# Performance work log

Measured on AMD Instinct MI355X. Metric: run time of the kernel, lower is better.

Reference implementation:

```python
import jax, jax.numpy as jnp
import numpy as np

B, S, D = 2, 2048, 2048
H = 16
Q_LORA = 1024
KV_LORA = 512
NOPE = 128
ROPE = 64
VH = 128
QK = NOPE + ROPE
EPS = 1e-3
SCALE = QK ** -0.5


def rms_norm(x, w):
    x32 = x.astype(jnp.float32)
    n = x32 * jax.lax.rsqrt(jnp.mean(x32 * x32, axis=-1, keepdims=True) + EPS)
    return w * n.astype(x.dtype)


def apply_rope(x, cos, sin):
    # x: [b, s, h, d]; cos/sin: [1, s, 1, d//2].
    # torch view_as_complex pairs consecutive elements: (x0,x1),(x2,x3),...
    xr, xi = x[..., 0::2], x[..., 1::2]
    yr = xr * cos - xi * sin
    yi = xr * sin + xi * cos
    return jnp.stack([yr, yi], axis=-1).reshape(x.shape)


def setup_inputs() -> dict:
    key = jax.random.key(0)
    ks = jax.random.split(key, 8)

    def lin(k, out, inn):
        bound = 1.0 / float(np.sqrt(inn))
        return jax.random.uniform(k, (out, inn), jnp.float32, -bound, bound)

    inv_freq = 1.0 / (10000.0 ** (np.arange(0, ROPE, 2, dtype=np.float32) / ROPE))
    ang = np.arange(S, dtype=np.float32)[:, None] * inv_freq[None, :]  # [S, ROPE/2]
    return {
        "x": jax.random.normal(ks[0], (B, S, D), jnp.float32),
        "start_pos": 0,
        "cos": jnp.asarray(np.cos(ang), jnp.float32),
        "sin": jnp.asarray(np.sin(ang), jnp.float32),
        "wq_a_w": lin(ks[1], Q_LORA, D),
        "wq_a_b": jnp.zeros((Q_LORA,), jnp.float32),
        "q_norm_w": jnp.ones((Q_LORA,), jnp.float32),
        "wq_b_w": lin(ks[2], H * QK, Q_LORA),
        "wq_b_b": jnp.zeros((H * QK,), jnp.float32),
        "wkv_a_w": lin(ks[3], KV_LORA + ROPE, D),
        "wkv_a_b": jnp.zeros((KV_LORA + ROPE,), jnp.float32),
        "kv_norm_w": jnp.ones((KV_LORA,), jnp.float32),
        "wkv_b_w": lin(ks[4], H * (NOPE + VH), KV_LORA),
        "wo_w": lin(ks[5], D, H * VH),
        "wo_b": jnp.zeros((D,), jnp.float32),
    }


def reference(x, start_pos, cos, sin, wq_a_w, wq_a_b, q_norm_w, wq_b_w, wq_b_b,
              wkv_a_w, wkv_a_b, kv_norm_w, wkv_b_w, wo_w, wo_b):
    b, s, _ = x.shape
    cos_ = cos[None, :, None, :]
    sin_ = sin[None, :, None, :]

    # q path: low-rank down-proj, RMSNorm, up-proj
    q = rms_norm(x @ wq_a_w.T + wq_a_b, q_norm_w) @ wq_b_w.T + wq_b_b
    q = q.reshape(b, s, H, QK)
    q_nope, q_pe = q[..., :NOPE], q[..., NOPE:]
    q_pe = apply_rope(q_pe, cos_, sin_)

    # kv path: joint low-rank latent + rope key
    kv_full = x @ wkv_a_w.T + wkv_a_b
    kv, k_pe = kv_full[..., :KV_LORA], kv_full[..., KV_LORA:]
    k_pe = apply_rope(k_pe[:, :, None, :], cos_, sin_)[:, :, 0, :]  # [b, t, ROPE]

    wkv_b = wkv_b_w.reshape(H, NOPE + VH, KV_LORA)
    # absorb k up-projection into q (MLA trick): q_nope -> latent space
    q_nope = jnp.einsum('bshd,hdc->bshc', q_nope, wkv_b[:, :NOPE])  # [b,s,H,KV_LORA]

    kv_c = rms_norm(kv, kv_norm_w)  # latent KV cache contents [b, t, KV_LORA]

    scores = (jnp.einsum('bshc,btc->bsht', q_nope, kv_c)
              + jnp.einsum('bshr,btr->bsht', q_pe, k_pe)) * SCALE
    # NOTE: source builds a causal mask but never adds it -> plain softmax (faithful)
    probs = jax.nn.softmax(scores.astype(jnp.float32), axis=-1).astype(x.dtype)

    o = jnp.einsum('bsht,btc->bshc', probs, kv_c)          # latent output
    o = jnp.einsum('bshc,hdc->bshd', o, wkv_b[:, NOPE:])    # v up-projection
    return o.reshape(b, s, H * VH) @ wo_w.T + wo_b
```

## Files before the change

kernel.cpp:

```cpp
#include <hip/hip_runtime.h>
#include <stdint.h>

typedef uint16_t u16;
typedef __bf16 bf16x8 __attribute__((ext_vector_type(8)));
typedef float f32x4 __attribute__((ext_vector_type(4)));
typedef u16 u16x8 __attribute__((ext_vector_type(8)));

#define EPS 1e-3f
#define SCALE_F 0.07216878364870323f
#define SCALE_L2E 0.104117546f
#define THR_RAW 110.0f

__device__ __forceinline__ float bf2f(u16 u) {
    union { uint32_t i; float f; } v; v.i = ((uint32_t)u) << 16; return v.f;
}
__device__ __forceinline__ u16 f2bf(float f) {
    union { float f; uint32_t i; } v; v.f = f;
    uint32_t x = v.i;
    return (u16)((x + 0x7fffu + ((x >> 16) & 1u)) >> 16);
}

__device__ __forceinline__ void async_cp16(const u16* g, u16* l) {
    __builtin_amdgcn_global_load_lds(
        (const __attribute__((address_space(1))) uint32_t*)g,
        (__attribute__((address_space(3))) uint32_t*)l,
        16, 0, 0);
}

struct Cvt {
    const void* src[14];
    u16* dst[14];
    long off[15];
};

__global__ __launch_bounds__(256) void cvt_kernel(Cvt c, const uint32_t* qnw_u32, long total8)
{
    const long i8 = (long)blockIdx.x * 256 + threadIdx.x;
    if (i8 >= total8) return;
    const long e = i8 * 8;
    const bool is_f32 = (qnw_u32[0] == 0x3F800000u);
    int t = 0;
    while (e >= c.off[t + 1]) ++t;
    const long local = e - c.off[t];
    u16* d = c.dst[t] + local;
    if (is_f32) {
        const float* s = (const float*)c.src[t] + local;
        const f32x4 a = *(const f32x4*)s;
        const f32x4 b = *(const f32x4*)(s + 4);
        u16x8 o;
        #pragma unroll
        for (int j = 0; j < 4; ++j) { o[j] = f2bf(a[j]); o[j + 4] = f2bf(b[j]); }
        *(u16x8*)d = o;
    } else {
        *(u16x8*)d = *(const u16x8*)((const u16*)c.src[t] + local);
    }
}

struct GemmP {
    const u16* A; const u16* B; const u16* bias; u16* C;
    int M, N, K, lda, ldb, ldc; float alpha; int c_f32;
    int z0, hcnt;
    long sAl, sAb, sAh, sBl, sBb, sBh, sCl, sCb, sCh;
    int gx, gy;
};

__device__ __forceinline__ void gemm_body(
    u16* As, u16* Bs, int bx, int by, int bz, const GemmP& p)
{
    const u16* A = p.A; const u16* B = p.B; const u16* bias = p.bias;
    u16* C = p.C;
    const int N = p.N, K = p.K, lda = p.lda, ldb = p.ldb, ldc = p.ldc;

    const int zg = p.z0 + bz;
    const int zb = zg / p.hcnt, zh = zg - zb * p.hcnt;
    A += (long)bz * p.sAl + (long)zb * p.sAb + (long)zh * p.sAh;
    B += (long)bz * p.sBl + (long)zb * p.sBb + (long)zh * p.sBh;
    C += (long)bz * p.sCl + (long)zb * p.sCb + (long)zh * p.sCh;

    const int tid  = threadIdx.x;
    const int wave = tid >> 6, lane = tid & 63;
    const int wm = (wave >> 1) << 6, wn = (wave & 1) << 6;
    const int quad = lane >> 4, r15 = lane & 15;

    const int tileM = by * 128;
    const int tileN = bx * 128;

    const u16* Ag[4]; const u16* Bg[4];
    u16* lA[4]; u16* lB[4];
    #pragma unroll
    for (int i = 0; i < 4; ++i) {
        const int cc = i * 256 + tid;
        const int rA = cc >> 3, kb = (cc & 7) << 3;
        int rB = tileN + rA; if (rB > N - 1) rB = N - 1;
        Ag[i] = A + (long)(tileM + rA) * lda + kb;
        Bg[i] = B + (long)rB * ldb + kb;
        lA[i] = &As[cc << 3];
        lB[i] = &Bs[cc << 3];
    }

    f32x4 acc[4][4] = {};

    const u16* aRd[4]; const u16* bRd[4];
    #pragma unroll
    for (int i = 0; i < 4; ++i) {
        aRd[i] = &As[(wm + i * 16 + r15) * 64 + quad * 8];
        bRd[i] = &Bs[(wn + i * 16 + r15) * 64 + quad * 8];
    }

    for (int k0 = 0; k0 < K; k0 += 64) {
        #pragma unroll
        for (int i = 0; i < 4; ++i) {
            async_cp16(Ag[i], lA[i]);
            async_cp16(Bg[i], lB[i]);
            Ag[i] += 64; Bg[i] += 64;
        }
        __syncthreads();
        #pragma unroll
        for (int kk = 0; kk < 2; ++kk) {
            bf16x8 af[4], bfr[4];
            #pragma unroll
            for (int i = 0; i < 4; ++i) {
                af[i]  = *(const bf16x8*)(aRd[i] + kk * 32);
                bfr[i] = *(const bf16x8*)(bRd[i] + kk * 32);
            }
            #pragma unroll
            for (int mi = 0; mi < 4; ++mi)
                #pragma unroll
                for (int ni = 0; ni < 4; ++ni)
                    acc[mi][ni] = __builtin_amdgcn_mfma_f32_16x16x32_bf16(
                        af[mi], bfr[ni], acc[mi][ni], 0, 0, 0);
        }
        __syncthreads();
    }

    #pragma unroll
    for (int mi = 0; mi < 4; ++mi) {
        const int row = tileM + wm + mi * 16 + quad * 4;
        #pragma unroll
        for (int ni = 0; ni < 4; ++ni) {
            const int col = tileN + wn + ni * 16 + r15;
            if (col < N) {
                if (p.c_f32) {
                    const float bv = bias ? bf2f(bias[col]) : 0.f;
                    #pragma unroll
                    for (int r = 0; r < 4; ++r)
                        ((float*)C)[(long)(row + r) * ldc + col] =
                            acc[mi][ni][r] * p.alpha + bv;
                } else {
                    #pragma unroll
                    for (int r = 0; r < 4; ++r) {
                        u16 t = f2bf(acc[mi][ni][r] * p.alpha);
                        if (bias) t = f2bf(bf2f(t) + bf2f(bias[col]));
                        C[(long)(row + r) * ldc + col] = t;
                    }
                }
            }
        }
    }
}

__global__ __launch_bounds__(256) void gemm_bt_kernel(GemmP p)
{
    __shared__ u16 As[128 * 64];
    __shared__ u16 Bs[128 * 64];
    gemm_body(As, Bs, blockIdx.x, blockIdx.y, blockIdx.z, p);
}

__global__ __launch_bounds__(256) void gemm_dual_kernel(GemmP pa, GemmP pb, int na)
{
    __shared__ u16 As[128 * 64];
    __shared__ u16 Bs[128 * 64];
    int bid = blockIdx.x;
    if (bid < na) {
        const int bx = bid % pa.gx; const int rem = bid / pa.gx;
        gemm_body(As, Bs, bx, rem % pa.gy, rem / pa.gy, pa);
    } else {
        bid -= na;
        const int bx = bid % pb.gx; const int rem = bid / pb.gx;
        gemm_body(As, Bs, bx, rem % pb.gy, rem / pb.gy, pb);
    }
}

#define PS 72

__global__ __launch_bounds__(256, 2) void flash_kernel(
    const u16* __restrict__ q, const u16* __restrict__ K2,
    const u16* __restrict__ Vt, u16* __restrict__ O,
    const u16* __restrict__ cosb, const u16* __restrict__ sinb)
{
    __shared__ __align__(16) u16 Ks[64 * 192];
    __shared__ __align__(16) u16 Vs[128 * 64];
    __shared__ __align__(16) u16 Ps[4][32 * PS];

    const int bid = blockIdx.x;
    const int xcd = bid & 7;
    const int idx = bid >> 3;
    const int bh  = xcd * 4 + (idx >> 4);
    const int mt  = idx & 15;
    const int b = bh >> 4, h = bh & 15;

    const int tid = threadIdx.x;
    const int wave = tid >> 6, lane = tid & 63;
    const int quad = lane >> 4, r15 = lane & 15;
    const int r7 = r15 & 7;

    const long qrow0 = (long)b * 2048 + mt * 128 + wave * 32;
    u16* myPs = Ps[wave];

    bf16x8 qf[2][6];
    #pragma unroll
    for (int mi = 0; mi < 2; ++mi) {
        const u16* qp = q + (qrow0 + mi * 16 + r15) * 3072 + h * 192 + quad * 8;
        #pragma unroll
        for (int kst = 0; kst < 4; ++kst)
            qf[mi][kst] = *(const bf16x8*)(qp + kst * 32);
        const int srow = mt * 128 + wave * 32 + mi * 16 + r15;
        #pragma unroll
        for (int kst = 4; kst < 6; ++kst) {
            const u16x8 v = *(const u16x8*)(qp + kst * 32);
            u16x8 o;
            const int jj0 = (kst - 4) * 16 + quad * 4;
            #pragma unroll
            for (int pp = 0; pp < 4; ++pp) {
                const float xr = bf2f(v[2 * pp]), xi = bf2f(v[2 * pp + 1]);
                const float c  = bf2f(cosb[(long)srow * 32 + jj0 + pp]);
                const float si = bf2f(sinb[(long)srow * 32 + jj0 + pp]);
                o[2 * pp]     = f2bf(bf2f(f2bf(xr * c))  - bf2f(f2bf(xi * si)));
                o[2 * pp + 1] = f2bf(bf2f(f2bf(xr * si)) + bf2f(f2bf(xi * c)));
            }
            qf[mi][kst] = *(const bf16x8*)&o;
        }
    }

    f32x4 Oacc[2][8] = {};
    float m_i[2][4], l_i[2][4];
    #pragma unroll
    for (int mi = 0; mi < 2; ++mi)
        #pragma unroll
        for (int r = 0; r < 4; ++r) { m_i[mi][r] = -1e30f; l_i[mi][r] = 0.f; }

    const u16* Kbh = K2 + (long)b * 2048 * 3072 + h * 192;
    const u16* Vbh = Vt + (long)bh * 128 * 2048;

    const u16* gK[6];
    #pragma unroll
    for (int i = 0; i < 6; ++i) {
        const int c = i * 256 + tid;
        const int row = c / 24, s = c - row * 24;
        gK[i] = Kbh + (long)row * 3072 + ((s ^ (row & 7)) << 3);
    }
    const u16* gV[4];
    #pragma unroll
    for (int i = 0; i < 4; ++i) {
        const int c = i * 256 + tid;
        const int d = c >> 3, s = c & 7;
        gV[i] = Vbh + (long)d * 2048 + ((s ^ (d & 7)) << 3);
    }

    #pragma unroll
    for (int i = 0; i < 6; ++i) {
        async_cp16(gK[i], &Ks[(i * 256 + tid) << 3]);
        gK[i] += 64 * 3072;
    }
    __syncthreads();

    for (int j = 0; j < 32; ++j) {
        #pragma unroll
        for (int i = 0; i < 4; ++i) {
            async_cp16(gV[i], &Vs[(i * 256 + tid) << 3]);
            gV[i] += 64;
        }

        f32x4 S[2][4] = {};
        __builtin_amdgcn_s_setprio(1);
        #pragma unroll
        for (int kst = 0; kst < 6; ++kst) {
            bf16x8 bfr[4];
            #pragma unroll
            for (int ni = 0; ni < 4; ++ni)
                bfr[ni] = *(const bf16x8*)&Ks[(ni * 16 + r15) * 192
                                              + (((kst * 4 + quad) ^ r7) << 3)];
            #pragma unroll
            for (int mi = 0; mi < 2; ++mi)
                #pragma unroll
                for (int ni = 0; ni < 4; ++ni)
                    S[mi][ni] = __builtin_amdgcn_mfma_f32_16x16x32_bf16(
                        qf[mi][kst], bfr[ni], S[mi][ni], 0, 0, 0);
        }
        __builtin_amdgcn_s_setprio(0);

        __syncthreads();

        #pragma unroll
        for (int i = 0; i < 6; ++i) {
            async_cp16(gK[i], &Ks[(i * 256 + tid) << 3]);
            gK[i] += 64 * 3072;
        }

        float tmax[2][4];
        float gmax = -1e30f;
        #pragma unroll
        for (int mi = 0; mi < 2; ++mi)
            #pragma unroll
            for (int r = 0; r < 4; ++r) {
                float t = fmaxf(fmaxf(S[mi][0][r], S[mi][1][r]),
                                fmaxf(S[mi][2][r], S[mi][3][r]));
                t = fmaxf(t, __shfl_xor(t, 1, 16));
                t = fmaxf(t, __shfl_xor(t, 2, 16));
                t = fmaxf(t, __shfl_xor(t, 4, 16));
                t = fmaxf(t, __shfl_xor(t, 8, 16));
                tmax[mi][r] = t;
                gmax = fmaxf(gmax, t - m_i[mi][r]);
            }
        if (!__all(gmax <= THR_RAW)) {
            #pragma unroll
            for (int mi = 0; mi < 2; ++mi)
                #pragma unroll
                for (int r = 0; r < 4; ++r) {
                    const float mnew = fmaxf(m_i[mi][r], tmax[mi][r]);
                    const float al = exp2f((m_i[mi][r] - mnew) * SCALE_L2E);
                    m_i[mi][r] = mnew;
                    l_i[mi][r] *= al;
                    #pragma unroll
                    for (int ni = 0; ni < 8; ++ni) Oacc[mi][ni][r] *= al;
                }
        }
        #pragma unroll
        for (int mi = 0; mi < 2; ++mi)
            #pragma unroll
            for (int r = 0; r < 4; ++r) {
                const int lrow = mi * 16 + quad * 4 + r;
                const float mm = m_i[mi][r];
                float ps = 0.f;
                #pragma unroll
                for (int ni = 0; ni < 4; ++ni) {
                    const float pv = exp2f((S[mi][ni][r] - mm) * SCALE_L2E);
                    ps += pv;
                    myPs[lrow * PS + ni * 16 + r15] = f2bf(pv);
                }
                ps += __shfl_xor(ps, 1, 16);
                ps += __shfl_xor(ps, 2, 16);
                ps += __shfl_xor(ps, 4, 16);
                ps += __shfl_xor(ps, 8, 16);
                l_i[mi][r] += ps;
            }

        __builtin_amdgcn_s_setprio(1);
        #pragma unroll
        for (int kst = 0; kst < 2; ++kst) {
            bf16x8 af[2], bv[8];
            #pragma unroll
            for (int mi = 0; mi < 2; ++mi)
                af[mi] = *(const bf16x8*)&myPs[(mi * 16 + r15) * PS
                                               + kst * 32 + quad * 8];
            #pragma unroll
            for (int ni = 0; ni < 8; ++ni)
                bv[ni] = *(const bf16x8*)&Vs[(ni * 16 + r15) * 64
                                             + (((kst * 4 + quad) ^ r7) << 3)];
            #pragma unroll
            for (int mi = 0; mi < 2; ++mi)
                #pragma unroll
                for (int ni = 0; ni < 8; ++ni)
                    Oacc[mi][ni] = __builtin_amdgcn_mfma_f32_16x16x32_bf16(
                        af[mi], bv[ni], Oacc[mi][ni], 0, 0, 0);
        }
        __builtin_amdgcn_s_setprio(0);

        __syncthreads();
    }

    #pragma unroll
    for (int mi = 0; mi < 2; ++mi)
        #pragma unroll
        for (int r = 0; r < 4; ++r) {
            const float inv = 1.f / l_i[mi][r];
            const long row = qrow0 + mi * 16 + quad * 4 + r;
            #pragma unroll
            for (int ni = 0; ni < 8; ++ni)
                O[row * 2048 + h * 128 + ni * 16 + r15] =
                    f2bf(Oacc[mi][ni][r] * inv);
        }
}

__global__ __launch_bounds__(256) void rmsnorm_kernel(
    const u16* __restrict__ x, const u16* __restrict__ w, u16* __restrict__ y,
    int n, int ldx)
{
    const long row = blockIdx.x;
    const u16* xr = x + row * ldx;
    u16* yr = y + row * ldx;
    const int tid = threadIdx.x;
    const int cnt = n >> 8;
    float v[4];
    float ss = 0.f;
    for (int i = 0; i < cnt; ++i) { v[i] = bf2f(xr[tid + (i << 8)]); ss += v[i] * v[i]; }
    for (int o = 32; o; o >>= 1) ss += __shfl_xor(ss, o, 64);
    __shared__ float sm[4];
    if ((tid & 63) == 0) sm[tid >> 6] = ss;
    __syncthreads();
    const float rinv = rsqrtf((sm[0] + sm[1] + sm[2] + sm[3]) / (float)n + EPS);
    for (int i = 0; i < cnt; ++i) {
        const u16 nb = f2bf(v[i] * rinv);
        yr[tid + (i << 8)] = f2bf(bf2f(w[tid + (i << 8)]) * bf2f(nb));
    }
}

__global__ __launch_bounds__(256) void kv_kernel(
    const u16* __restrict__ cosb, const u16* __restrict__ sinb,
    const u16* __restrict__ w, u16* __restrict__ comb, u16* __restrict__ K2)
{
    const long bs = blockIdx.x;
    const int s = (int)(bs & 2047);
    u16* io = comb + bs * 1600 + 1024;
    const int tid = threadIdx.x;
    const float v0 = bf2f(io[tid * 2]), v1 = bf2f(io[tid * 2 + 1]);
    float ss = v0 * v0 + v1 * v1;
    for (int off = 32; off; off >>= 1) ss += __shfl_xor(ss, off, 64);
    __shared__ float sm[4];
    __shared__ u16 rp[64];
    if ((tid & 63) == 0) sm[tid >> 6] = ss;
    __syncthreads();
    const float rinv = rsqrtf((sm[0] + sm[1] + sm[2] + sm[3]) / 512.f + EPS);
    const u16 n0 = f2bf(v0 * rinv), n1 = f2bf(v1 * rinv);
    io[tid * 2]     = f2bf(bf2f(w[tid * 2]) * bf2f(n0));
    io[tid * 2 + 1] = f2bf(bf2f(w[tid * 2 + 1]) * bf2f(n1));
    if (tid < 32) {
        const int j = tid;
        const float xr = bf2f(io[512 + 2 * j]), xi = bf2f(io[512 + 2 * j + 1]);
        const float c = bf2f(cosb[s * 32 + j]), si = bf2f(sinb[s * 32 + j]);
        rp[2 * j]     = f2bf(bf2f(f2bf(xr * c))  - bf2f(f2bf(xi * si)));
        rp[2 * j + 1] = f2bf(bf2f(f2bf(xr * si)) + bf2f(f2bf(xi * c)));
    }
    __syncthreads();
    #pragma unroll
    for (int i = 0; i < 4; ++i) {
        const int slot = tid + (i << 8);
        const int h = slot >> 6, r = slot & 63;
        K2[bs * 3072 + h * 192 + 128 + r] = rp[r];
    }
}

extern "C" void kernel_launch(void* const* d_in, const int* in_sizes, int n_in,
                              void* d_out, int out_size, void* d_ws, size_t ws_size,
                              hipStream_t stream)
{
    float* out = (float*)d_out;

    char* p = (char*)d_ws;
    auto alloc = [&](size_t elems) { u16* r = (u16*)p; p += elems * 2; return r; };
    u16* c_cos  = alloc(65536);
    u16* c_sin  = alloc(65536);
    u16* c_wqa  = alloc(2097152);
    u16* c_wkva = alloc(1179648);
    u16* c_wqab = alloc(1024);
    u16* c_wkvab= alloc(576);
    u16* c_qnw  = alloc(1024);
    u16* c_wqb  = alloc(3145728);
    u16* c_wqbb = alloc(3072);
    u16* c_kvnw = alloc(512);
    u16* c_wkvb = alloc(2097152);
    u16* c_wo   = alloc(4194304);
    u16* c_wob  = alloc(2048);
    u16* q    = alloc(4096UL * 3072);
    u16* K2   = alloc(4096UL * 3072);
    u16* O    = alloc(4096UL * 2048);
    u16* comb = alloc(4096UL * 1600);
    u16* xb = (u16*)d_out;
    u16* Vt = (u16*)d_out + 8388608;

    Cvt cv;
    const long sizes[14] = {8388608, 65536, 65536, 2097152, 1024, 1024, 3145728,
                            3072, 1179648, 576, 512, 2097152, 4194304, 2048};
    u16* dsts[14] = {xb, c_cos, c_sin, c_wqa, c_wqab, c_qnw, c_wqb, c_wqbb,
                     c_wkva, c_wkvab, c_kvnw, c_wkvb, c_wo, c_wob};
    const int srcidx[14] = {0, 2, 3, 4, 5, 6, 7, 8, 9, 10, 11, 12, 13, 14};
    long acc_off = 0;
    for (int t = 0; t < 14; ++t) {
        cv.src[t] = d_in[srcidx[t]];
        cv.dst[t] = dsts[t];
        cv.off[t] = acc_off;
        acc_off += sizes[t];
    }
    cv.off[14] = acc_off;
    const long total8 = acc_off / 8;
    cvt_kernel<<<dim3((unsigned)((total8 + 255) / 256)), dim3(256), 0, stream>>>(
        cv, (const uint32_t*)d_in[6], total8);

    auto mkp = [&](const u16* A, const u16* B, const u16* bias, u16* C,
                   int M, int N, int K, int lda, int ldb, int ldc, float alpha,
                   int c_f32, int z0, int hcnt,
                   long sAl, long sAb, long sAh,
                   long sBl, long sBb, long sBh,
                   long sCl, long sCb, long sCh) {
        GemmP g;
        g.A = A; g.B = B; g.bias = bias; g.C = C;
        g.M = M; g.N = N; g.K = K; g.lda = lda; g.ldb = ldb; g.ldc = ldc;
        g.alpha = alpha; g.c_f32 = c_f32; g.z0 = z0; g.hcnt = hcnt;
        g.sAl = sAl; g.sAb = sAb; g.sAh = sAh;
        g.sBl = sBl; g.sBb = sBb; g.sBh = sBh;
        g.sCl = sCl; g.sCb = sCb; g.sCh = sCh;
        g.gx = (N + 127) / 128; g.gy = M / 128;
        return g;
    };
    auto gemm = [&](const GemmP& g, int nz) {
        gemm_bt_kernel<<<dim3(g.gx, g.gy, nz), dim3(256), 0, stream>>>(g);
    };

    gemm(mkp(xb, c_wqa, c_wqab, comb, 4096, 1600, 2048, 2048, 2048, 1600, 1.f, 0,
             0, 1, 0, 0, 0, 0, 0, 0, 0, 0, 0), 1);
    rmsnorm_kernel<<<4096, 256, 0, stream>>>(comb, c_qnw, comb, 1024, 1600);
    gemm(mkp(comb, c_wqb, c_wqbb, q, 4096, 3072, 1024, 1600, 1024, 3072, 1.f, 0,
             0, 1, 0, 0, 0, 0, 0, 0, 0, 0, 0), 1);
    kv_kernel<<<4096, 256, 0, stream>>>(c_cos, c_sin, c_kvnw, comb, K2);
    {
        GemmP pk = mkp(comb + 1024, c_wkvb, nullptr, K2,
                       4096, 128, 512, 1600, 512, 3072, 1.f, 0,
                       0, 16, 0, 0, 0, 0, 0, 256L * 512, 0, 0, 192);
        pk.gx = 1; pk.gy = 32;
        GemmP pv = mkp(c_wkvb + 128 * 512, comb + 1024, nullptr, Vt,
                       128, 2048, 512, 512, 1600, 2048, 1.f, 0,
                       0, 16,
                       0, 0, 256L * 512,
                       0, 2048L * 1600, 0,
                       0, 16L * 128 * 2048, 128L * 2048);
        pv.gx = 16; pv.gy = 1;
        gemm_dual_kernel<<<dim3(1024), dim3(256), 0, stream>>>(pk, pv, 512);
    }
    flash_kernel<<<dim3(512), dim3(256), 0, stream>>>(q, K2, Vt, O, c_cos, c_sin);
    gemm(mkp(O, c_wo, c_wob, (u16*)out, 4096, 2048, 2048, 2048, 2048, 2048, 1.f, 1,
             0, 1, 0, 0, 0, 0, 0, 0, 0, 0, 0), 1);
}
```

Measured before the change: 532.7 us.

## Merge q/kv norm kernels and batch wq_b GEMM with k/v absorb GEMMs

The separate q RMSNorm and kv norm+rope kernels are fused into a single launch that covers 8192 blocks. The wq_b up-projection GEMM now runs in one three-way grouped GEMM launch together with the k-absorb and v GEMMs. The aim is fewer launches and better CU fill for the small GEMMs. Separately, the flash softmax now uses __expf with the natural scale instead of exp2f with a pre-multiplied log2e scale. That may cost an extra multiply inside __expf.

```diff
diff --git a/kernel.cpp b/kernel.cpp
--- a/kernel.cpp
+++ b/kernel.cpp
@@ -8,7 +8,6 @@
 
 #define EPS 1e-3f
 #define SCALE_F 0.07216878364870323f
-#define SCALE_L2E 0.104117546f
 #define THR_RAW 110.0f
 
 __device__ __forceinline__ float bf2f(u16 u) {
@@ -166,7 +165,8 @@
     gemm_body(As, Bs, blockIdx.x, blockIdx.y, blockIdx.z, p);
 }
 
-__global__ __launch_bounds__(256) void gemm_dual_kernel(GemmP pa, GemmP pb, int na)
+__global__ __launch_bounds__(256) void gemm_tri_kernel(
+    GemmP pa, GemmP pb, GemmP pc, int na, int nb)
 {
     __shared__ u16 As[128 * 64];
     __shared__ u16 Bs[128 * 64];
@@ -174,10 +174,14 @@
     if (bid < na) {
         const int bx = bid % pa.gx; const int rem = bid / pa.gx;
         gemm_body(As, Bs, bx, rem % pa.gy, rem / pa.gy, pa);
-    } else {
+    } else if (bid < na + nb) {
         bid -= na;
         const int bx = bid % pb.gx; const int rem = bid / pb.gx;
         gemm_body(As, Bs, bx, rem % pb.gy, rem / pb.gy, pb);
+    } else {
+        bid -= na + nb;
+        const int bx = bid % pc.gx; const int rem = bid / pc.gx;
+        gemm_body(As, Bs, bx, rem % pc.gy, rem / pc.gy, pc);
     }
 }
 
@@ -303,8 +307,9 @@
         for (int mi = 0; mi < 2; ++mi)
             #pragma unroll
             for (int r = 0; r < 4; ++r) {
-                float t = fmaxf(fmaxf(S[mi][0][r], S[mi][1][r]),
-                                fmaxf(S[mi][2][r], S[mi][3][r]));
+                float t = S[mi][0][r];
+                #pragma unroll
+                for (int ni = 1; ni < 4; ++ni) t = fmaxf(t, S[mi][ni][r]);
                 t = fmaxf(t, __shfl_xor(t, 1, 16));
                 t = fmaxf(t, __shfl_xor(t, 2, 16));
                 t = fmaxf(t, __shfl_xor(t, 4, 16));
@@ -318,7 +323,7 @@
                 #pragma unroll
                 for (int r = 0; r < 4; ++r) {
                     const float mnew = fmaxf(m_i[mi][r], tmax[mi][r]);
-                    const float al = exp2f((m_i[mi][r] - mnew) * SCALE_L2E);
+                    const float al = __expf((m_i[mi][r] - mnew) * SCALE_F);
                     m_i[mi][r] = mnew;
                     l_i[mi][r] *= al;
                     #pragma unroll
@@ -334,7 +339,7 @@
                 float ps = 0.f;
                 #pragma unroll
                 for (int ni = 0; ni < 4; ++ni) {
-                    const float pv = exp2f((S[mi][ni][r] - mm) * SCALE_L2E);
+                    const float pv = __expf((S[mi][ni][r] - mm) * SCALE_F);
                     ps += pv;
                     myPs[lrow * PS + ni * 16 + r15] = f2bf(pv);
                 }
@@ -382,61 +387,57 @@
         }
 }
 
-__global__ __launch_bounds__(256) void rmsnorm_kernel(
-    const u16* __restrict__ x, const u16* __restrict__ w, u16* __restrict__ y,
-    int n, int ldx)
-{
-    const long row = blockIdx.x;
-    const u16* xr = x + row * ldx;
-    u16* yr = y + row * ldx;
-    const int tid = threadIdx.x;
-    const int cnt = n >> 8;
-    float v[4];
-    float ss = 0.f;
-    for (int i = 0; i < cnt; ++i) { v[i] = bf2f(xr[tid + (i << 8)]); ss += v[i] * v[i]; }
-    for (int o = 32; o; o >>= 1) ss += __shfl_xor(ss, o, 64);
-    __shared__ float sm[4];
-    if ((tid & 63) == 0) sm[tid >> 6] = ss;
-    __syncthreads();
-    const float rinv = rsqrtf((sm[0] + sm[1] + sm[2] + sm[3]) / (float)n + EPS);
-    for (int i = 0; i < cnt; ++i) {
-        const u16 nb = f2bf(v[i] * rinv);
-        yr[tid + (i << 8)] = f2bf(bf2f(w[tid + (i << 8)]) * bf2f(nb));
-    }
-}
-
-__global__ __launch_bounds__(256) void kv_kernel(
+__global__ __launch_bounds__(256) void norm_kv_kernel(
     const u16* __restrict__ cosb, const u16* __restrict__ sinb,
-    const u16* __restrict__ w, u16* __restrict__ comb, u16* __restrict__ K2)
-{
-    const long bs = blockIdx.x;
-    const int s = (int)(bs & 2047);
-    u16* io = comb + bs * 1600 + 1024;
-    const int tid = threadIdx.x;
-    const float v0 = bf2f(io[tid * 2]), v1 = bf2f(io[tid * 2 + 1]);
-    float ss = v0 * v0 + v1 * v1;
-    for (int off = 32; off; off >>= 1) ss += __shfl_xor(ss, off, 64);
+    const u16* __restrict__ qnw, const u16* __restrict__ kvnw,
+    u16* __restrict__ comb, u16* __restrict__ K2)
+{
     __shared__ float sm[4];
     __shared__ u16 rp[64];
-    if ((tid & 63) == 0) sm[tid >> 6] = ss;
-    __syncthreads();
-    const float rinv = rsqrtf((sm[0] + sm[1] + sm[2] + sm[3]) / 512.f + EPS);
-    const u16 n0 = f2bf(v0 * rinv), n1 = f2bf(v1 * rinv);
-    io[tid * 2]     = f2bf(bf2f(w[tid * 2]) * bf2f(n0));
-    io[tid * 2 + 1] = f2bf(bf2f(w[tid * 2 + 1]) * bf2f(n1));
-    if (tid < 32) {
-        const int j = tid;
-        const float xr = bf2f(io[512 + 2 * j]), xi = bf2f(io[512 + 2 * j + 1]);
-        const float c = bf2f(cosb[s * 32 + j]), si = bf2f(sinb[s * 32 + j]);
-        rp[2 * j]     = f2bf(bf2f(f2bf(xr * c))  - bf2f(f2bf(xi * si)));
-        rp[2 * j + 1] = f2bf(bf2f(f2bf(xr * si)) + bf2f(f2bf(xi * c)));
-    }
-    __syncthreads();
-    #pragma unroll
-    for (int i = 0; i < 4; ++i) {
-        const int slot = tid + (i << 8);
-        const int h = slot >> 6, r = slot & 63;
-        K2[bs * 3072 + h * 192 + 128 + r] = rp[r];
+    const int bid = blockIdx.x;
+    const int tid = threadIdx.x;
+    if (bid < 4096) {
+        u16* xr = comb + (long)bid * 1600;
+        float v[4];
+        float ss = 0.f;
+        #pragma unroll
+        for (int i = 0; i < 4; ++i) { v[i] = bf2f(xr[tid + (i << 8)]); ss += v[i] * v[i]; }
+        for (int o = 32; o; o >>= 1) ss += __shfl_xor(ss, o, 64);
+        if ((tid & 63) == 0) sm[tid >> 6] = ss;
+        __syncthreads();
+        const float rinv = rsqrtf((sm[0] + sm[1] + sm[2] + sm[3]) / 1024.f + EPS);
+        #pragma unroll
+        for (int i = 0; i < 4; ++i) {
+            const u16 nb = f2bf(v[i] * rinv);
+            xr[tid + (i << 8)] = f2bf(bf2f(qnw[tid + (i << 8)]) * bf2f(nb));
+        }
+    } else {
+        const long bs = bid - 4096;
+        const int s = (int)(bs & 2047);
+        u16* io = comb + bs * 1600 + 1024;
+        const float v0 = bf2f(io[tid * 2]), v1 = bf2f(io[tid * 2 + 1]);
+        float ss = v0 * v0 + v1 * v1;
+        for (int off = 32; off; off >>= 1) ss += __shfl_xor(ss, off, 64);
+        if ((tid & 63) == 0) sm[tid >> 6] = ss;
+        __syncthreads();
+        const float rinv = rsqrtf((sm[0] + sm[1] + sm[2] + sm[3]) / 512.f + EPS);
+        const u16 n0 = f2bf(v0 * rinv), n1 = f2bf(v1 * rinv);
+        io[tid * 2]     = f2bf(bf2f(kvnw[tid * 2]) * bf2f(n0));
+        io[tid * 2 + 1] = f2bf(bf2f(kvnw[tid * 2 + 1]) * bf2f(n1));
+        if (tid < 32) {
+            const int j = tid;
+            const float xr = bf2f(io[512 + 2 * j]), xi = bf2f(io[512 + 2 * j + 1]);
+            const float c = bf2f(cosb[s * 32 + j]), si = bf2f(sinb[s * 32 + j]);
+            rp[2 * j]     = f2bf(bf2f(f2bf(xr * c))  - bf2f(f2bf(xi * si)));
+            rp[2 * j + 1] = f2bf(bf2f(f2bf(xr * si)) + bf2f(f2bf(xi * c)));
+        }
+        __syncthreads();
+        #pragma unroll
+        for (int i = 0; i < 4; ++i) {
+            const int slot = tid + (i << 8);
+            const int h = slot >> 6, r = slot & 63;
+            K2[bs * 3072 + h * 192 + 128 + r] = rp[r];
+        }
     }
 }
 
@@ -508,11 +509,12 @@
 
     gemm(mkp(xb, c_wqa, c_wqab, comb, 4096, 1600, 2048, 2048, 2048, 1600, 1.f, 0,
              0, 1, 0, 0, 0, 0, 0, 0, 0, 0, 0), 1);
-    rmsnorm_kernel<<<4096, 256, 0, stream>>>(comb, c_qnw, comb, 1024, 1600);
-    gemm(mkp(comb, c_wqb, c_wqbb, q, 4096, 3072, 1024, 1600, 1024, 3072, 1.f, 0,
-             0, 1, 0, 0, 0, 0, 0, 0, 0, 0, 0), 1);
-    kv_kernel<<<4096, 256, 0, stream>>>(c_cos, c_sin, c_kvnw, comb, K2);
+    norm_kv_kernel<<<dim3(8192), dim3(256), 0, stream>>>(
+        c_cos, c_sin, c_qnw, c_kvnw, comb, K2);
     {
+        GemmP pq = mkp(comb, c_wqb, c_wqbb, q,
+                       4096, 3072, 1024, 1600, 1024, 3072, 1.f, 0,
+                       0, 1, 0, 0, 0, 0, 0, 0, 0, 0, 0);
         GemmP pk = mkp(comb + 1024, c_wkvb, nullptr, K2,
                        4096, 128, 512, 1600, 512, 3072, 1.f, 0,
                        0, 16, 0, 0, 0, 0, 0, 256L * 512, 0, 0, 192);
@@ -524,7 +526,7 @@
                        0, 2048L * 1600, 0,
                        0, 16L * 128 * 2048, 128L * 2048);
         pv.gx = 16; pv.gy = 1;
-        gemm_dual_kernel<<<dim3(1024), dim3(256), 0, stream>>>(pk, pv, 512);
+        gemm_tri_kernel<<<dim3(1792), dim3(256), 0, stream>>>(pq, pk, pv, 768, 512);
     }
     flash_kernel<<<dim3(512), dim3(256), 0, stream>>>(q, K2, Vt, O, c_cos, c_sin);
     gemm(mkp(O, c_wo, c_wob, (u16*)out, 4096, 2048, 2048, 2048, 2048, 2048, 1.f, 1,
```

After: 500.2 us. -6.1%, faster.
